# Performance work log

Hardware: AMD Instinct MI355X
Metric: run time of the kernel (lower is better)

## Reference

```python
import jax, jax.numpy as jnp
import numpy as np

NUM_GROUPS = 2          # ['dark_skin', 'light_skin']
NUM_SUBGROUPS = 6       # 2 skin tones x 3 classes
NUM_CLASSES = 3
BAL_ACC_W = 0.3         # GroupDROConfig.BALANCED_ACCURACY_WEIGHT
BRIGHTNESS_THRESH = 0.4 # _estimate_skin_tone_from_image threshold

N = 16777216


def setup_inputs() -> dict:
    key = jax.random.key(0)
    k1, k2 = jax.random.split(key)
    logits = jax.random.normal(k1, (N, NUM_CLASSES), dtype=jnp.float32)
    labels = jax.random.randint(k2, (N,), 0, NUM_CLASSES, dtype=jnp.int32)
    group_weights = jnp.ones((NUM_GROUPS,), dtype=jnp.float32)  # buffer init
    return {"logits": logits, "labels": labels, "group_weights": group_weights}


def reference(logits, labels, group_weights):
    # per-sample cross entropy (reduction='none')
    log_probs = jax.nn.log_softmax(logits, axis=-1)              # [N, C]
    ce = -jnp.take_along_axis(log_probs, labels[:, None], axis=-1)[:, 0]  # [N]

    # group assignment: forward passes logits as 'images'; fallback brightness
    # estimate is mean over the sample; < 0.4 -> dark (idx 0) else light (idx 1)
    brightness = jnp.mean(logits, axis=-1)                        # [N]
    group_idx = jnp.where(brightness < BRIGHTNESS_THRESH, 0, 1).astype(jnp.int32)
    subgroup_idx = group_idx * NUM_CLASSES + labels               # [N], in [0,6)

    # scatter-add (segment reduce) of per-sample CE into group / subgroup bins
    group_losses = jax.ops.segment_sum(ce, group_idx, num_segments=NUM_GROUPS)
    subgroup_losses = jax.ops.segment_sum(ce, subgroup_idx, num_segments=NUM_SUBGROUPS)

    # weighted worst-group style aggregation
    total_loss = jnp.sum(group_losses * group_weights)
    standard_loss = jnp.mean(ce)  # F.cross_entropy default mean reduction
    combined_loss = (1.0 - BAL_ACC_W) * standard_loss + BAL_ACC_W * total_loss
    return combined_loss, group_losses, subgroup_losses
```

## Files before the change

kernel.cpp:

```cpp
#include <hip/hip_runtime.h>


constexpr int N_SAMPLES = 16777216;
constexpr int NQ = N_SAMPLES / 4;
constexpr int BLOCK = 256;
constexpr int GRID = 1024;
constexpr int STRIDE = GRID * BLOCK;
constexpr int ITERS = NQ / STRIDE;
constexpr int WAVES = BLOCK / 64;

static_assert(ITERS * STRIDE == NQ, "exact tiling");

__global__ __launch_bounds__(BLOCK) void dro_partial(
    const float* __restrict__ logits,
    const int*   __restrict__ labels,
    float*       __restrict__ partials)
{
    const float4* __restrict__ lg = (const float4*)logits;
    const int4*   __restrict__ lb = (const int4*)labels;

    float acc[6] = {0.f, 0.f, 0.f, 0.f, 0.f, 0.f};
    const int base = blockIdx.x * BLOCK + threadIdx.x;

    #pragma unroll 2
    for (int it = 0; it < ITERS; ++it) {
        const int q = base + it * STRIDE;
        float4 p0 = lg[3 * q + 0];
        float4 p1 = lg[3 * q + 1];
        float4 p2 = lg[3 * q + 2];
        int4   l4 = lb[q];

        float xs[12] = {p0.x, p0.y, p0.z, p0.w, p1.x, p1.y,
                        p1.z, p1.w, p2.x, p2.y, p2.z, p2.w};
        int   ls[4]  = {l4.x, l4.y, l4.z, l4.w};

        #pragma unroll
        for (int s = 0; s < 4; ++s) {
            float a = xs[3 * s], b = xs[3 * s + 1], c = xs[3 * s + 2];
            int lab = ls[s];

            float m  = fmaxf(a, fmaxf(b, c));
            float ea = __expf(a - m), eb = __expf(b - m), ec = __expf(c - m);
            float lse = m + __logf(ea + eb + ec);
            float xl = (lab == 0) ? a : ((lab == 1) ? b : c);
            float ce = lse - xl;

            float mean = (a + b + c) * (1.0f / 3.0f);
            int g  = (mean < 0.4f) ? 0 : 1;
            int sg = g * 3 + lab;

            #pragma unroll
            for (int j = 0; j < 6; ++j)
                acc[j] += (j == sg) ? ce : 0.0f;
        }
    }

    #pragma unroll
    for (int j = 0; j < 6; ++j) {
        #pragma unroll
        for (int off = 32; off > 0; off >>= 1)
            acc[j] += __shfl_down(acc[j], off, 64);
    }

    __shared__ float lds[WAVES][6];
    const int wave = threadIdx.x >> 6;
    const int lane = threadIdx.x & 63;
    if (lane == 0) {
        #pragma unroll
        for (int j = 0; j < 6; ++j) lds[wave][j] = acc[j];
    }
    __syncthreads();

    if (threadIdx.x < 6) {
        float s = 0.f;
        #pragma unroll
        for (int w = 0; w < WAVES; ++w) s += lds[w][threadIdx.x];
        partials[blockIdx.x * 6 + threadIdx.x] = s;
    }
}

__global__ __launch_bounds__(BLOCK) void dro_finalize(
    const float* __restrict__ partials,
    const float* __restrict__ gw,
    float* __restrict__ out)
{
    float acc[6] = {0.f, 0.f, 0.f, 0.f, 0.f, 0.f};
    for (int b = threadIdx.x; b < GRID; b += BLOCK) {
        #pragma unroll
        for (int j = 0; j < 6; ++j) acc[j] += partials[b * 6 + j];
    }

    #pragma unroll
    for (int j = 0; j < 6; ++j) {
        #pragma unroll
        for (int off = 32; off > 0; off >>= 1)
            acc[j] += __shfl_down(acc[j], off, 64);
    }

    __shared__ float lds[WAVES][6];
    const int wave = threadIdx.x >> 6;
    const int lane = threadIdx.x & 63;
    if (lane == 0) {
        #pragma unroll
        for (int j = 0; j < 6; ++j) lds[wave][j] = acc[j];
    }
    __syncthreads();

    if (threadIdx.x == 0) {
        float sg[6];
        float tot = 0.f;
        #pragma unroll
        for (int j = 0; j < 6; ++j) {
            float s = 0.f;
            #pragma unroll
            for (int w = 0; w < WAVES; ++w) s += lds[w][j];
            sg[j] = s;
            tot += s;
        }
        float g0 = sg[0] + sg[1] + sg[2];
        float g1 = sg[3] + sg[4] + sg[5];
        float total_loss = g0 * gw[0] + g1 * gw[1];
        float standard   = tot / (float)N_SAMPLES;
        float combined   = 0.7f * standard + 0.3f * total_loss;
        out[0] = combined;
        out[1] = g0;
        out[2] = g1;
        #pragma unroll
        for (int j = 0; j < 6; ++j) out[3 + j] = sg[j];
    }
}

extern "C" void kernel_launch(void* const* d_in, const int* in_sizes, int n_in,
                              void* d_out, int out_size, void* d_ws, size_t ws_size,
                              hipStream_t stream) {
    const float* logits = (const float*)d_in[0];
    const int*   labels = (const int*)d_in[1];
    const float* gw     = (const float*)d_in[2];
    float* partials = (float*)d_ws;
    float* out      = (float*)d_out;

    dro_partial<<<GRID, BLOCK, 0, stream>>>(logits, labels, partials);
    dro_finalize<<<1, BLOCK, 0, stream>>>(partials, gw, out);
}
```

Baseline: 319.8 us.

## Stage logits and labels through LDS with double-buffered async global loads

Replaces the per-thread strided float4 global loads with coalesced 16-byte `global_load_lds` copies into a double-buffered LDS tile. The next iteration is prefetched while the current one is computed. Each thread then reads its 12 logits and 4 labels from LDS. The aim is better coalescing and more memory requests in flight. The cost is a block barrier every iteration, possible LDS bank conflicts from the 48-byte per-thread stride, and reliance on the compiler emitting correct vmcnt waits before the barrier.

```diff
diff --git a/kernel.cpp b/kernel.cpp
--- a/kernel.cpp
+++ b/kernel.cpp
@@ -1,4 +1,5 @@
 #include <hip/hip_runtime.h>
+#include <stdint.h>
 
 
 constexpr int N_SAMPLES = 16777216;
@@ -11,41 +12,67 @@
 
 static_assert(ITERS * STRIDE == NQ, "exact tiling");
 
+#define GLOBAL_AS __attribute__((address_space(1)))
+#define LDS_AS    __attribute__((address_space(3)))
+
+__device__ __forceinline__ void async_copy16(const void* g, void* l) {
+    __builtin_amdgcn_global_load_lds((const GLOBAL_AS void*)g,
+                                     (LDS_AS void*)l, 16, 0, 0);
+}
+
 __global__ __launch_bounds__(BLOCK) void dro_partial(
     const float* __restrict__ logits,
     const int*   __restrict__ labels,
     float*       __restrict__ partials)
 {
-    const float4* __restrict__ lg = (const float4*)logits;
-    const int4*   __restrict__ lb = (const int4*)labels;
+    __shared__ float4 slog[2][3 * BLOCK];
+    __shared__ int4   slab[2][BLOCK];
+
+    const float4* __restrict__ lgq = (const float4*)logits;
+    const int4*   __restrict__ lbq = (const int4*)labels;
+
+    const int t = threadIdx.x;
+    const int b = blockIdx.x;
+
+    auto stage = [&](int it, int buf) {
+        const int qbase  = it * STRIDE + b * BLOCK;
+        const int f4base = 3 * qbase;
+        #pragma unroll
+        for (int k = 0; k < 3; ++k)
+            async_copy16(&lgq[f4base + k * BLOCK + t], &slog[buf][k * BLOCK + t]);
+        async_copy16(&lbq[qbase + t], &slab[buf][t]);
+    };
 
     float acc[6] = {0.f, 0.f, 0.f, 0.f, 0.f, 0.f};
-    const int base = blockIdx.x * BLOCK + threadIdx.x;
 
-    #pragma unroll 2
+    stage(0, 0);
     for (int it = 0; it < ITERS; ++it) {
-        const int q = base + it * STRIDE;
-        float4 p0 = lg[3 * q + 0];
-        float4 p1 = lg[3 * q + 1];
-        float4 p2 = lg[3 * q + 2];
-        int4   l4 = lb[q];
+        __syncthreads();
+        if (it + 1 < ITERS) stage(it + 1, (it + 1) & 1);
 
-        float xs[12] = {p0.x, p0.y, p0.z, p0.w, p1.x, p1.y,
-                        p1.z, p1.w, p2.x, p2.y, p2.z, p2.w};
+        const int buf = it & 1;
+        const float* xs = (const float*)&slog[buf][0];
+        float4 v0 = *(const float4*)&xs[12 * t + 0];
+        float4 v1 = *(const float4*)&xs[12 * t + 4];
+        float4 v2 = *(const float4*)&xs[12 * t + 8];
+        int4   l4 = slab[buf][t];
+
+        float fs[12] = {v0.x, v0.y, v0.z, v0.w, v1.x, v1.y,
+                        v1.z, v1.w, v2.x, v2.y, v2.z, v2.w};
         int   ls[4]  = {l4.x, l4.y, l4.z, l4.w};
 
         #pragma unroll
         for (int s = 0; s < 4; ++s) {
-            float a = xs[3 * s], b = xs[3 * s + 1], c = xs[3 * s + 2];
+            float a = fs[3 * s], bb = fs[3 * s + 1], c = fs[3 * s + 2];
             int lab = ls[s];
 
-            float m  = fmaxf(a, fmaxf(b, c));
-            float ea = __expf(a - m), eb = __expf(b - m), ec = __expf(c - m);
+            float m  = fmaxf(a, fmaxf(bb, c));
+            float ea = __expf(a - m), eb = __expf(bb - m), ec = __expf(c - m);
             float lse = m + __logf(ea + eb + ec);
-            float xl = (lab == 0) ? a : ((lab == 1) ? b : c);
+            float xl = (lab == 0) ? a : ((lab == 1) ? bb : c);
             float ce = lse - xl;
 
-            float mean = (a + b + c) * (1.0f / 3.0f);
+            float mean = (a + bb + c) * (1.0f / 3.0f);
             int g  = (mean < 0.4f) ? 0 : 1;
             int sg = g * 3 + lab;
 
@@ -62,19 +89,20 @@
             acc[j] += __shfl_down(acc[j], off, 64);
     }
 
-    __shared__ float lds[WAVES][6];
+    __shared__ float red[WAVES][6];
     const int wave = threadIdx.x >> 6;
     const int lane = threadIdx.x & 63;
+    __syncthreads();
     if (lane == 0) {
         #pragma unroll
-        for (int j = 0; j < 6; ++j) lds[wave][j] = acc[j];
+        for (int j = 0; j < 6; ++j) red[wave][j] = acc[j];
     }
     __syncthreads();
 
     if (threadIdx.x < 6) {
         float s = 0.f;
         #pragma unroll
-        for (int w = 0; w < WAVES; ++w) s += lds[w][threadIdx.x];
+        for (int w = 0; w < WAVES; ++w) s += red[w][threadIdx.x];
         partials[blockIdx.x * 6 + threadIdx.x] = s;
     }
 }
@@ -97,12 +125,12 @@
             acc[j] += __shfl_down(acc[j], off, 64);
     }
 
-    __shared__ float lds[WAVES][6];
+    __shared__ float red[WAVES][6];
     const int wave = threadIdx.x >> 6;
     const int lane = threadIdx.x & 63;
     if (lane == 0) {
         #pragma unroll
-        for (int j = 0; j < 6; ++j) lds[wave][j] = acc[j];
+        for (int j = 0; j < 6; ++j) red[wave][j] = acc[j];
     }
     __syncthreads();
 
@@ -113,7 +141,7 @@
         for (int j = 0; j < 6; ++j) {
             float s = 0.f;
             #pragma unroll
-            for (int w = 0; w < WAVES; ++w) s += lds[w][j];
+            for (int w = 0; w < WAVES; ++w) s += red[w][j];
             sg[j] = s;
             tot += s;
         }
```

After: 320.2 us. No clear change (+0.1%).
